# Performance work log

Hardware: AMD Instinct MI355X
Metric: run time of the kernel (lower is better)

## Reference

```python
import jax, jax.numpy as jnp
import numpy as np

H = W = 128
HW = H * W
BIG = HW  # sentinel label for background (also serves as the background 'component' id, like cv2 label 0)


def _neighbor_min(L2):
    # min over 8-connected neighborhood + self (cv2 default connectivity=8)
    Lp = jnp.pad(L2, 1, constant_values=BIG)
    m = L2
    for dr in (-1, 0, 1):
        for dc in (-1, 0, 1):
            m = jnp.minimum(m, Lp[1 + dr:1 + dr + H, 1 + dc:1 + dc + W])
    return m


def _cc_labels(fg):
    """Connected-component labeling via min-label propagation + pointer jumping.
    fg: (H,W) bool. Returns (HW,) int32: each fg pixel gets the min flat index
    of its component; bg pixels get BIG."""
    idx = jnp.arange(HW, dtype=jnp.int32)
    L0 = jnp.where(fg.reshape(-1), idx, jnp.int32(BIG))

    def step(L):
        L2 = jnp.where(fg, L.reshape(H, W), jnp.int32(BIG))
        m = jnp.where(fg, _neighbor_min(L2), jnp.int32(BIG)).reshape(-1)
        # two pointer-jumps (path compression) for fast convergence
        ext = jnp.append(m, jnp.int32(BIG))
        m = ext[m]
        m = jnp.append(m, jnp.int32(BIG))[m]
        return m

    def cond(st):
        return st[1]

    def body(st):
        L, _ = st
        Ln = step(L)
        return (Ln, jnp.any(Ln != L))

    L, _ = jax.lax.while_loop(cond, body, (L0, jnp.bool_(True)))
    return L


def _mask_loss(mask):
    # mask: (H, W) float. Faithful to torch: components computed on detached mask.
    fg = jax.lax.stop_gradient(mask) > 0
    L = _cc_labels(fg)  # (HW,) labels in [0, HW]; BIG == background component
    flat = jnp.arange(HW, dtype=jnp.int32)
    rows = flat // W
    cols = flat % W
    n = HW + 1
    area = jax.ops.segment_sum(jnp.ones(HW, jnp.int32), L, num_segments=n)
    rmin = jax.ops.segment_min(rows, L, num_segments=n)
    rmax = jax.ops.segment_max(rows, L, num_segments=n)
    cmin = jax.ops.segment_min(cols, L, num_segments=n)
    cmax = jax.ops.segment_max(cols, L, num_segments=n)
    a = jnp.where(area > 0, area, -1)
    top2_vals, top2_idx = jax.lax.top_k(a, 2)
    have2 = top2_vals[1] > 0  # len(stats) > 1 in the original
    j = top2_idx[1]           # second-largest-area component (stats[-2])
    r0, r1, c0, c1 = rmin[j], rmax[j], cmin[j], cmax[j]
    rr = jnp.arange(H)[:, None]
    cc = jnp.arange(W)[None, :]
    inbox = (rr >= r0) & (rr <= r1) & (cc >= c0) & (cc <= c1) & have2
    pmask = jnp.where(inbox, jnp.zeros((), mask.dtype), jnp.ones((), mask.dtype))
    return (pmask * mask).mean()


def setup_inputs() -> dict:
    key = jax.random.key(0)
    masks = jax.random.normal(key, (8, 16, H, W), dtype=jnp.float32)
    return {"masks": masks}


def reference(masks):
    b, k, h, w = masks.shape
    flat = masks.reshape(b * k, h, w)
    losses = jax.vmap(_mask_loss)(flat)
    return losses.mean()
```

## Files before the change

kernel.cpp:

```cpp
#include <hip/hip_runtime.h>
#include <hip/hip_bf16.h>
#include <stdint.h>

#define HH 128
#define WW 128
#define HWPX 16384
#define BIGL 16384
#define NT 1024
#define PPT 16

__device__ __forceinline__ int findRootH(int* L, int x) {
    int p = L[x];
    while (p != x) {
        int g = L[p];
        if (g != p) atomicMin(&L[x], g);
        x = p; p = g;
    }
    return x;
}
__device__ __forceinline__ int findRootF(int* L, int x) {
    int p = L[x];
    while (p != x) {
        int g = L[p];
        if (g != p) L[x] = g;
        x = p; p = g;
    }
    return p;
}
__device__ __forceinline__ void uni(int* L, int a, int b) {
    a = findRootH(L, a);
    b = findRootH(L, b);
    while (a != b) {
        if (a > b) { int t = a; a = b; b = t; }
        int old = atomicMin(&L[b], a);
        if (old == b) break;
        b = old;
    }
}

__device__ __forceinline__ int wsumi(int v)    { for (int o = 32; o; o >>= 1) v += __shfl_xor(v, o, 64); return v; }
__device__ __forceinline__ float wsumf(float v){ for (int o = 32; o; o >>= 1) v += __shfl_xor(v, o, 64); return v; }
__device__ __forceinline__ int wmini(int v)    { for (int o = 32; o; o >>= 1) v = min(v, __shfl_xor(v, o, 64)); return v; }
__device__ __forceinline__ int wmaxi(int v)    { for (int o = 32; o; o >>= 1) v = max(v, __shfl_xor(v, o, 64)); return v; }

__global__ __launch_bounds__(NT)
void cc_kernel(const float* __restrict__ masks, float* __restrict__ losses) {
    __shared__ int L[HWPX];
    __shared__ unsigned rowbits[HH][4];
    __shared__ int s_bg;
    __shared__ int s_r0, s_r1, s_c0, s_c1;
    __shared__ unsigned s_k2;
    __shared__ unsigned s_wk[32];
    __shared__ float s_wsum[16];
    __shared__ float s_total;

    const int tid = threadIdx.x;
    const int lane = tid & 63;
    const int wid = tid >> 6;
    const float* msk = masks + (size_t)blockIdx.x * HWPX;
    const int base = tid * PPT;
    const int row  = base >> 7;
    const int col0 = base & 127;

    float vals[PPT];
    const float4* m4 = (const float4*)(msk + base);
#pragma unroll
    for (int q = 0; q < 4; ++q) {
        float4 v = m4[q];
        vals[q * 4 + 0] = v.x; vals[q * 4 + 1] = v.y;
        vals[q * 4 + 2] = v.z; vals[q * 4 + 3] = v.w;
    }
    unsigned fgbits = 0;
    float tsum = 0.f;
    int lab[PPT];
    {
        int start = -1;
#pragma unroll
        for (int k = 0; k < PPT; ++k) {
            tsum += vals[k];
            if (vals[k] > 0.f) {
                fgbits |= 1u << k;
                if (start < 0) start = k;
                lab[k] = base + start;
            } else {
                start = -1;
                lab[k] = BIGL;
            }
        }
    }
    {
        int4* Lv = (int4*)(L + base);
#pragma unroll
        for (int q = 0; q < 4; ++q)
            Lv[q] = make_int4(lab[q * 4], lab[q * 4 + 1], lab[q * 4 + 2], lab[q * 4 + 3]);
    }
    unsigned lf = __shfl(fgbits, lane > 0 ? lane - 1 : lane, 64);
    unsigned rf = __shfl(fgbits, lane < 63 ? lane + 1 : lane, 64);
    const unsigned leftbit  = (col0 > 0)   ? ((lf >> 15) & 1u) : 0u;
    const unsigned rightbit = (col0 < 112) ? (rf & 1u)         : 0u;
    unsigned other = __shfl_xor(fgbits, 1, 64);
    if (!(tid & 1)) rowbits[row][(tid >> 1) & 3] = fgbits | (other << 16);

    tsum = wsumf(tsum);
    if (lane == 0) s_wsum[wid] = tsum;
    if (tid == 0) { s_bg = 0; s_r0 = HH; s_r1 = -1; s_c0 = WW; s_c1 = -1; }
    __syncthreads();

    if (tid < 64) {
        float t = (tid < 16) ? s_wsum[tid] : 0.f;
        for (int o = 8; o; o >>= 1) t += __shfl_xor(t, o, 64);
        if (tid == 0) s_total = t;
    }
    if (fgbits) {
        unsigned up = 0;
        if (row > 0) {
            const int wi  = col0 >> 5;
            const int off = col0 & 31;
            unsigned w0 = rowbits[row - 1][wi];
            unsigned w1 = (wi < 3) ? rowbits[row - 1][wi + 1] : 0u;
            unsigned long long uv = ((unsigned long long)w1 << 32) | w0;
            if (off == 16) {
                up = (unsigned)(uv >> 15) & 0x3FFFFu;
            } else {
                unsigned lw = (col0 > 0) ? rowbits[row - 1][wi - 1] : 0u;
                up = (unsigned)((uv << 1) | (lw >> 31)) & 0x3FFFFu;
            }
        }
        if ((fgbits & 1u) && leftbit) uni(L, base, base - 1);
        const unsigned ULv = up & 0xFFFFu;
        const unsigned UPv = (up >> 1) & 0xFFFFu;
        const unsigned URv = (up >> 2) & 0xFFFFu;
        const unsigned lFv = ((fgbits << 1) | leftbit) & 0xFFFFu;
        const unsigned rFv = (fgbits >> 1) | (rightbit << 15);
        unsigned m = fgbits & ( (~lFv & (ULv | UPv | URv))
                              | (lFv & ((UPv & ~ULv) | (~rFv & URv & ~UPv))) );
        while (m) {
            int k = __ffs(m) - 1; m &= m - 1;
            unsigned t = ~fgbits & ((1u << k) - 1u);
            int head = base + (t ? (32 - __builtin_clz(t)) : 0);
            unsigned UL = (ULv >> k) & 1u;
            unsigned UP = (UPv >> k) & 1u;
            unsigned UR = (URv >> k) & 1u;
            unsigned lF = (lFv >> k) & 1u;
            unsigned rF = (rFv >> k) & 1u;
            int i = base + k;
            if (!lF) {
                if (UL)        uni(L, head, i - WW - 1);
                if (UP && !UL) uni(L, head, i - WW);
                if (UR && !UP) uni(L, head, i - WW + 1);
            } else {
                if (UP && !UL)        uni(L, head, i - WW);
                if (!rF && UR && !UP) uni(L, head, i - WW + 1);
            }
        }
    }
    __syncthreads();

    int rr[PPT];
    int firstRoot = 0x7FFFFFFF;
    {
        int cur = -1;
#pragma unroll
        for (int k = 0; k < PPT; ++k) {
            rr[k] = -1;
            if (fgbits & (1u << k)) {
                if (k == 0 || !(fgbits & (1u << (k - 1)))) {
                    cur = findRootF(L, base + k);
                    L[base + k] = cur;
                }
                rr[k] = cur;
                if (firstRoot == 0x7FFFFFFF) firstRoot = cur;
            }
        }
    }
    __syncthreads();

    {
        const int R0 = wmini(firstRoot);
        int giant = 0, bgc = 0, prev = -1, cnt = 0;
#pragma unroll
        for (int k = 0; k < PPT; ++k) {
            if (!(fgbits & (1u << k))) { ++bgc; continue; }
            int r = rr[k];
            if (r == R0) { ++giant; }
            else if (r == prev) ++cnt;
            else {
                if (cnt) atomicAdd(&L[prev], cnt << 16);
                prev = r; cnt = 1;
            }
        }
        if (cnt) atomicAdd(&L[prev], cnt << 16);
        int g = wsumi(giant);
        if (lane == 0 && R0 != 0x7FFFFFFF && g) atomicAdd(&L[R0], g << 16);
        int b = wsumi(bgc);
        if (lane == 0 && b) atomicAdd(&s_bg, b);
    }
    __syncthreads();

    int bg = s_bg;
    unsigned b1 = 0, b2 = 0;
    if (tid == 0 && bg > 0) b1 = ((unsigned)bg << 15);
    {
        unsigned m = fgbits & ~(fgbits << 1);
        while (m) {
            int k = __ffs(m) - 1; m &= m - 1;
            int h = base + k;
            int e = L[h];
            if ((e & 0xFFFF) == h && (e >> 16) != 0) {
                unsigned key = ((unsigned)(e >> 16) << 15) | (unsigned)(BIGL - h);
                if (key > b1) { b2 = b1; b1 = key; }
                else if (key > b2) b2 = key;
            }
        }
    }
    for (int o = 32; o; o >>= 1) {
        unsigned p1 = __shfl_xor(b1, o, 64);
        unsigned p2 = __shfl_xor(b2, o, 64);
        if (p1 > b1) { b2 = (b1 > p2 ? b1 : p2); b1 = p1; }
        else if (p1 > b2) b2 = p1;
    }
    if (lane == 0) { s_wk[wid * 2] = b1; s_wk[wid * 2 + 1] = b2; }
    __syncthreads();
    if (tid < 64) {
        unsigned o1 = (tid < 16) ? s_wk[tid * 2] : 0u;
        unsigned o2 = (tid < 16) ? s_wk[tid * 2 + 1] : 0u;
        for (int o = 8; o; o >>= 1) {
            unsigned p1 = __shfl_xor(o1, o, 64);
            unsigned p2 = __shfl_xor(o2, o, 64);
            if (p1 > o1) { o2 = (o1 > p2 ? o1 : p2); o1 = p1; }
            else if (p1 > o2) o2 = p1;
        }
        if (tid == 0) s_k2 = o2;
    }
    __syncthreads();

    unsigned k2 = s_k2;
    bool have2 = (k2 >> 15) != 0;
    int j = BIGL - (int)(k2 & 0x7FFFu);

    if (have2) {
        int lc0 = WW, lc1 = -1;
#pragma unroll
        for (int k = 0; k < PPT; ++k) {
            bool inc = (fgbits & (1u << k)) ? (rr[k] == j) : (j == BIGL);
            if (inc) {
                int c = col0 + k;
                lc0 = min(lc0, c); lc1 = max(lc1, c);
            }
        }
        int lr0 = (lc1 >= 0) ? row : HH;
        int lr1 = (lc1 >= 0) ? row : -1;
        lr0 = wmini(lr0); lr1 = wmaxi(lr1);
        lc0 = wmini(lc0); lc1 = wmaxi(lc1);
        if (lane == 0 && lr1 >= 0) {
            atomicMin(&s_r0, lr0); atomicMax(&s_r1, lr1);
            atomicMin(&s_c0, lc0); atomicMax(&s_c1, lc1);
        }
    }
    __syncthreads();

    float bsum = 0.f;
    if (have2) {
        int r0 = s_r0, r1 = s_r1, c0 = s_c0, c1 = s_c1;
        if (row >= r0 && row <= r1) {
#pragma unroll
            for (int k = 0; k < PPT; ++k) {
                int c = col0 + k;
                if (c >= c0 && c <= c1) bsum += vals[k];
            }
        }
    }
    bsum = wsumf(bsum);
    if (lane == 0) s_wsum[wid] = bsum;
    __syncthreads();
    if (tid < 64) {
        float t = (tid < 16) ? s_wsum[tid] : 0.f;
        for (int o = 8; o; o >>= 1) t += __shfl_xor(t, o, 64);
        if (tid == 0) losses[blockIdx.x] = (s_total - t) * (1.0f / 16384.0f);
    }
}

__global__ void reduce_kernel(const float* __restrict__ losses, float* __restrict__ out, int n) {
    __shared__ float s[4];
    int t = threadIdx.x;
    float v = 0.f;
    for (int i = t; i < n; i += 256) v += losses[i];
    for (int off = 32; off; off >>= 1) v += __shfl_down(v, off, 64);
    if ((t & 63) == 0) s[t >> 6] = v;
    __syncthreads();
    if (t == 0) out[0] = (s[0] + s[1] + s[2] + s[3]) / (float)n;
}

extern "C" void kernel_launch(void* const* d_in, const int* in_sizes, int n_in,
                              void* d_out, int out_size, void* d_ws, size_t ws_size,
                              hipStream_t stream) {
    const float* masks = (const float*)d_in[0];
    float* out = (float*)d_out;
    float* losses = (float*)d_ws;
    int nmask = in_sizes[0] / HWPX;
    cc_kernel<<<nmask, NT, 0, stream>>>(masks, losses);
    reduce_kernel<<<1, 256, 0, stream>>>(losses, out, nmask);
}
```

Before: 47.15 us.

## Fold final mean into last block and drop intermediate barrier phases

The background count is now derived from a per-wave popcount of foreground bits instead of an atomic counter. The top-2 selection and the total-sum reduction are done redundantly by each thread straight from shared per-wave partials, which removes two barrier-plus-single-wave reduction phases. The separate reduce kernel is replaced by a last-block-done pattern using a global atomic counter and padded per-block loss slots, at the cost of a memset launch and a serial loop over 128 values in one thread. The fallback path, used when the workspace is too small, passes the workspace base as the counter, which aliases the first loss slot.

```diff
diff --git a/kernel.cpp b/kernel.cpp
--- a/kernel.cpp
+++ b/kernel.cpp
@@ -8,6 +8,7 @@
 #define BIGL 16384
 #define NT 1024
 #define PPT 16
+#define LSTRIDE 32
 
 __device__ __forceinline__ int findRootH(int* L, int x) {
     int p = L[x];
@@ -44,15 +45,15 @@
 __device__ __forceinline__ int wmaxi(int v)    { for (int o = 32; o; o >>= 1) v = max(v, __shfl_xor(v, o, 64)); return v; }
 
 __global__ __launch_bounds__(NT)
-void cc_kernel(const float* __restrict__ masks, float* __restrict__ losses) {
+void cc_kernel(const float* __restrict__ masks, float* __restrict__ lossP,
+               int* __restrict__ counter, float* __restrict__ out) {
     __shared__ int L[HWPX];
     __shared__ unsigned rowbits[HH][4];
-    __shared__ int s_bg;
     __shared__ int s_r0, s_r1, s_c0, s_c1;
-    __shared__ unsigned s_k2;
     __shared__ unsigned s_wk[32];
-    __shared__ float s_wsum[16];
-    __shared__ float s_total;
+    __shared__ int s_wi[16];
+    __shared__ float s_wA[16];
+    __shared__ float s_wB[16];
 
     const int tid = threadIdx.x;
     const int lane = tid & 63;
@@ -102,15 +103,11 @@
     if (!(tid & 1)) rowbits[row][(tid >> 1) & 3] = fgbits | (other << 16);
 
     tsum = wsumf(tsum);
-    if (lane == 0) s_wsum[wid] = tsum;
-    if (tid == 0) { s_bg = 0; s_r0 = HH; s_r1 = -1; s_c0 = WW; s_c1 = -1; }
-    __syncthreads();
-
-    if (tid < 64) {
-        float t = (tid < 16) ? s_wsum[tid] : 0.f;
-        for (int o = 8; o; o >>= 1) t += __shfl_xor(t, o, 64);
-        if (tid == 0) s_total = t;
-    }
+    int fgc = wsumi(__popc(fgbits));
+    if (lane == 0) { s_wA[wid] = tsum; s_wi[wid] = fgc; }
+    if (tid == 0) { s_r0 = HH; s_r1 = -1; s_c0 = WW; s_c1 = -1; }
+    __syncthreads();
+
     if (fgbits) {
         unsigned up = 0;
         if (row > 0) {
@@ -177,12 +174,12 @@
 
     {
         const int R0 = wmini(firstRoot);
-        int giant = 0, bgc = 0, prev = -1, cnt = 0;
+        int giant = 0, prev = -1, cnt = 0;
 #pragma unroll
         for (int k = 0; k < PPT; ++k) {
-            if (!(fgbits & (1u << k))) { ++bgc; continue; }
+            if (!(fgbits & (1u << k))) continue;
             int r = rr[k];
-            if (r == R0) { ++giant; }
+            if (r == R0) ++giant;
             else if (r == prev) ++cnt;
             else {
                 if (cnt) atomicAdd(&L[prev], cnt << 16);
@@ -192,14 +189,10 @@
         if (cnt) atomicAdd(&L[prev], cnt << 16);
         int g = wsumi(giant);
         if (lane == 0 && R0 != 0x7FFFFFFF && g) atomicAdd(&L[R0], g << 16);
-        int b = wsumi(bgc);
-        if (lane == 0 && b) atomicAdd(&s_bg, b);
-    }
-    __syncthreads();
-
-    int bg = s_bg;
+    }
+    __syncthreads();
+
     unsigned b1 = 0, b2 = 0;
-    if (tid == 0 && bg > 0) b1 = ((unsigned)bg << 15);
     {
         unsigned m = fgbits & ~(fgbits << 1);
         while (m) {
@@ -221,22 +214,24 @@
     }
     if (lane == 0) { s_wk[wid * 2] = b1; s_wk[wid * 2 + 1] = b2; }
     __syncthreads();
-    if (tid < 64) {
-        unsigned o1 = (tid < 16) ? s_wk[tid * 2] : 0u;
-        unsigned o2 = (tid < 16) ? s_wk[tid * 2 + 1] : 0u;
-        for (int o = 8; o; o >>= 1) {
-            unsigned p1 = __shfl_xor(o1, o, 64);
-            unsigned p2 = __shfl_xor(o2, o, 64);
-            if (p1 > o1) { o2 = (o1 > p2 ? o1 : p2); o1 = p1; }
-            else if (p1 > o2) o2 = p1;
-        }
-        if (tid == 0) s_k2 = o2;
-    }
-    __syncthreads();
-
-    unsigned k2 = s_k2;
-    bool have2 = (k2 >> 15) != 0;
-    int j = BIGL - (int)(k2 & 0x7FFFu);
+
+    unsigned g1 = 0, g2 = 0;
+    {
+        int fgtot = 0;
+#pragma unroll
+        for (int w = 0; w < 16; ++w) fgtot += s_wi[w];
+        int bg = HWPX - fgtot;
+        if (bg > 0) g1 = (unsigned)bg << 15;
+#pragma unroll
+        for (int w = 0; w < 16; ++w) {
+            unsigned o1 = s_wk[w * 2], o2 = s_wk[w * 2 + 1];
+            if (o1 > g1) { g2 = (g1 > o2 ? g1 : o2); g1 = o1; }
+            else if (o1 > g2) g2 = o1;
+        }
+    }
+    const unsigned k2 = g2;
+    const bool have2 = (k2 >> 15) != 0;
+    const int j = BIGL - (int)(k2 & 0x7FFFu);
 
     if (have2) {
         int lc0 = WW, lc1 = -1;
@@ -271,12 +266,23 @@
         }
     }
     bsum = wsumf(bsum);
-    if (lane == 0) s_wsum[wid] = bsum;
-    __syncthreads();
-    if (tid < 64) {
-        float t = (tid < 16) ? s_wsum[tid] : 0.f;
-        for (int o = 8; o; o >>= 1) t += __shfl_xor(t, o, 64);
-        if (tid == 0) losses[blockIdx.x] = (s_total - t) * (1.0f / 16384.0f);
+    if (lane == 0) s_wB[wid] = bsum;
+    __syncthreads();
+
+    if (tid == 0) {
+        float tot = 0.f, bx = 0.f;
+#pragma unroll
+        for (int w = 0; w < 16; ++w) { tot += s_wA[w]; bx += s_wB[w]; }
+        lossP[(size_t)blockIdx.x * LSTRIDE] = (tot - bx) * (1.0f / 16384.0f);
+        __threadfence();
+        int old = atomicAdd(counter, 1);
+        if (old == (int)gridDim.x - 1) {
+            __threadfence();
+            float s = 0.f;
+            const volatile float* lp = (const volatile float*)lossP;
+            for (int i = 0; i < (int)gridDim.x; ++i) s += lp[(size_t)i * LSTRIDE];
+            out[0] = s / (float)gridDim.x;
+        }
     }
 }
 
@@ -284,7 +290,7 @@
     __shared__ float s[4];
     int t = threadIdx.x;
     float v = 0.f;
-    for (int i = t; i < n; i += 256) v += losses[i];
+    for (int i = t; i < n; i += 256) v += losses[i * LSTRIDE];
     for (int off = 32; off; off >>= 1) v += __shfl_down(v, off, 64);
     if ((t & 63) == 0) s[t >> 6] = v;
     __syncthreads();
@@ -296,8 +302,16 @@
                               hipStream_t stream) {
     const float* masks = (const float*)d_in[0];
     float* out = (float*)d_out;
-    float* losses = (float*)d_ws;
     int nmask = in_sizes[0] / HWPX;
-    cc_kernel<<<nmask, NT, 0, stream>>>(masks, losses);
-    reduce_kernel<<<1, 256, 0, stream>>>(losses, out, nmask);
-}
+    float* lossP = (float*)d_ws;
+    size_t lossB = (size_t)nmask * LSTRIDE * sizeof(float);
+    int* counter = (int*)((char*)d_ws + lossB);
+    size_t need = lossB + sizeof(int);
+    if (ws_size >= need) {
+        hipMemsetAsync(counter, 0, sizeof(int), stream);
+        cc_kernel<<<nmask, NT, 0, stream>>>(masks, lossP, counter, out);
+    } else {
+        cc_kernel<<<nmask, NT, 0, stream>>>(masks, lossP, (int*)d_ws, out);
+        reduce_kernel<<<1, 256, 0, stream>>>(lossP, out, nmask);
+    }
+}
```

Result: slower. 79.55 us, median of 2 (+68.7%).
